# Performance work log

Measured on AMD Instinct MI355X. Metric: run time of the kernel, lower is better.

The kernel has to match this reference:

```python
import jax, jax.numpy as jnp
import numpy as np

N_DRUG = 50000
N_PROT = 50000
E = 1000000
H = 128

def setup_inputs() -> dict:
    key = jax.random.key(0)
    k1, k2, k3, k4, k5 = jax.random.split(key, 5)
    z_drug = jax.random.normal(k1, (N_DRUG, H), dtype=jnp.float32)
    z_protein = jax.random.normal(k2, (N_PROT, H), dtype=jnp.float32)
    edge_label_index = jax.random.randint(k3, (2, E), 0, N_DRUG, dtype=jnp.int64)
    # Linear params (Kaiming-ish scale)
    W1 = jax.random.normal(k4, (H, 2 * H), dtype=jnp.float32) / np.sqrt(2 * H)
    b1 = jnp.zeros((H,), dtype=jnp.float32)
    W2 = jax.random.normal(k5, (1, H), dtype=jnp.float32) / np.sqrt(H)
    b2 = jnp.zeros((1,), dtype=jnp.float32)
    return {"z_drug": z_drug, "z_protein": z_protein,
            "edge_label_index": edge_label_index,
            "W1": W1, "b1": b1, "W2": W2, "b2": b2}

def reference(z_drug, z_protein, edge_label_index, W1, b1, W2, b2):
    row, col = edge_label_index[0], edge_label_index[1]
    # gather node embeddings along edges, concat -> [E, 2H]
    z = jnp.concatenate([z_drug[row], z_protein[col]], axis=-1)
    h = jax.nn.relu(jnp.einsum('eh,oh->eo', z, W1) + b1)  # [E, H]
    out = jnp.einsum('eh,oh->eo', h, W2) + b2             # [E, 1]
    return out.reshape(-1)
```

## Files before the change

### kernel.cpp

```cpp
#include <hip/hip_runtime.h>


typedef __attribute__((ext_vector_type(8))) short bhalf8;
typedef __attribute__((ext_vector_type(4))) float f32x4;
typedef _Float16 half2_t __attribute__((ext_vector_type(2)));

__device__ __forceinline__ unsigned bfr(float f) {
    unsigned u = __builtin_bit_cast(unsigned, f);
    return (u + 0x7fffu + ((u >> 16) & 1u)) >> 16;
}
__device__ __forceinline__ unsigned pk2(float a, float b) {
    return bfr(a) | (bfr(b) << 16);
}

#define SH_STRIDE 132

__global__ __launch_bounds__(512) void hprepq_kernel(
    const float* __restrict__ zd, const float* __restrict__ zp,
    const float* __restrict__ W1, const float* __restrict__ b1,
    unsigned char* __restrict__ Hd, unsigned char* __restrict__ Hp,
    float* __restrict__ scD, float* __restrict__ scP,
    int Nd, int Np, int nbd)
{
    __shared__ __align__(16) char smem[64 * SH_STRIDE * 4];
    short* sZ = (short*)smem;
    float* sH = (float*)smem;

    const bool isP = (int)blockIdx.x >= nbd;
    const float* z = isP ? zp : zd;
    unsigned char* H = isP ? Hp : Hd;
    float* sc = isP ? scP : scD;
    const int N    = isP ? Np : Nd;
    const int koff = isP ? 128 : 0;
    const int blk  = isP ? blockIdx.x - nbd : blockIdx.x;

    const int tid  = threadIdx.x;
    const int wave = tid >> 6;
    const int lane = tid & 63;
    const int l15  = lane & 15;
    const int lhi  = lane >> 4;
    const int ocol = wave * 16 + l15;

    bhalf8 bfrag[4];
    #pragma unroll
    for (int ks = 0; ks < 4; ++ks) {
        const float4* src = (const float4*)(W1 + ocol * 256 + koff + ks * 32 + lhi * 8);
        float4 p = src[0], q = src[1];
        bhalf8 f;
        f[0] = (short)bfr(p.x); f[1] = (short)bfr(p.y);
        f[2] = (short)bfr(p.z); f[3] = (short)bfr(p.w);
        f[4] = (short)bfr(q.x); f[5] = (short)bfr(q.y);
        f[6] = (short)bfr(q.z); f[7] = (short)bfr(q.w);
        bfrag[ks] = f;
    }
    const float bias = isP ? 0.0f : b1[ocol];
    const int r0 = blk * 64;

    {
        const int rl = tid >> 3;
        const int grow = min(r0 + rl, N - 1);
        const float4* zr = (const float4*)(z + (size_t)grow * 128);
        #pragma unroll
        for (int q = 0; q < 4; ++q) {
            const int s = (tid & 7) + q * 8;
            float4 v = zr[s];
            uint2 w; w.x = pk2(v.x, v.y); w.y = pk2(v.z, v.w);
            int byte = (rl * 256 + s * 8) ^ ((rl & 7) << 4);
            *(uint2*)((char*)sZ + byte) = w;
        }
    }
    __syncthreads();

    f32x4 acc[4] = {{0.f,0.f,0.f,0.f},{0.f,0.f,0.f,0.f},
                    {0.f,0.f,0.f,0.f},{0.f,0.f,0.f,0.f}};
    #pragma unroll
    for (int ks = 0; ks < 4; ++ks) {
        #pragma unroll
        for (int rt = 0; rt < 4; ++rt) {
            const int row = rt * 16 + l15;
            int byte = (row * 256 + ks * 64 + lhi * 16) ^ ((row & 7) << 4);
            bhalf8 af = *(const bhalf8*)((const char*)sZ + byte);
            acc[rt] = __builtin_amdgcn_mfma_f32_16x16x32_bf16(af, bfrag[ks], acc[rt], 0, 0, 0);
        }
    }
    __syncthreads();

    #pragma unroll
    for (int rt = 0; rt < 4; ++rt) {
        #pragma unroll
        for (int i = 0; i < 4; ++i) {
            const int row = rt * 16 + lhi * 4 + i;
            sH[row * SH_STRIDE + ocol] = acc[rt][i] + bias;
        }
    }
    __syncthreads();

    {
        const int qrow = tid >> 3;
        const int k    = tid & 7;
        float4 v4[4];
        float mx = 0.0f;
        #pragma unroll
        for (int j = 0; j < 4; ++j) {
            v4[j] = *(const float4*)(sH + qrow * SH_STRIDE + k * 16 + j * 4);
            mx = fmaxf(mx, fmaxf(fmaxf(fabsf(v4[j].x), fabsf(v4[j].y)),
                                 fmaxf(fabsf(v4[j].z), fabsf(v4[j].w))));
        }
        mx = fmaxf(mx, __shfl_xor(mx, 1, 64));
        mx = fmaxf(mx, __shfl_xor(mx, 2, 64));
        mx = fmaxf(mx, __shfl_xor(mx, 4, 64));
        const float inv = 127.0f / fmaxf(mx, 1e-20f);
        uint4 o;
        unsigned ob[4];
        #pragma unroll
        for (int j = 0; j < 4; ++j) {
            int a0 = __float2int_rn(v4[j].x * inv);
            int a1 = __float2int_rn(v4[j].y * inv);
            int a2 = __float2int_rn(v4[j].z * inv);
            int a3 = __float2int_rn(v4[j].w * inv);
            ob[j] = ((unsigned)(a0 & 0xff) | ((unsigned)(a1 & 0xff) << 8) |
                     ((unsigned)(a2 & 0xff) << 16) | ((unsigned)(a3 & 0xff) << 24))
                    ^ 0x80808080u;
        }
        o.x = ob[0]; o.y = ob[1]; o.z = ob[2]; o.w = ob[3];
        const int grow = r0 + qrow;
        if (grow < N) {
            *(uint4*)(H + (size_t)grow * 128 + k * 16) = o;
            if (k == 0) sc[grow] = mx * (1.0f / 127.0f);
        }
    }
}

__global__ __launch_bounds__(256, 4) void edgeq_kernel(
    const unsigned char* __restrict__ Hd, const unsigned char* __restrict__ Hp,
    const float* __restrict__ scD, const float* __restrict__ scP,
    const int* __restrict__ eli, const float* __restrict__ W2,
    const float* __restrict__ b2, float* __restrict__ out, int E)
{
    const int sub = threadIdx.x & 7;
    const int grp = threadIdx.x >> 3;
    half2_t w2h[8];
    #pragma unroll
    for (int j = 0; j < 8; ++j) {
        float2 w = ((const float2*)W2)[sub * 8 + j];
        w2h[j][0] = (_Float16)w.x; w2h[j][1] = (_Float16)w.y;
    }
    const float b2v = b2[0];
    const half2_t c1152 = { (_Float16)1152.0f, (_Float16)1152.0f };

    const int EPB = 32 * 4;
    const int step = gridDim.x * EPB;
    int base = blockIdx.x * EPB;
    if (base >= E) return;

    int row[4], col[4];
    #pragma unroll
    for (int u = 0; u < 4; ++u) {
        const int e = base + grp * 4 + u;
        row[u] = (e < E) ? eli[e] : 0;
        col[u] = (e < E) ? eli[E + e] : 0;
    }

    for (; base < E; base += step) {
        uint4 qd[4], qp[4];
        float sdc[4], r[4];
        #pragma unroll
        for (int u = 0; u < 4; ++u) {
            qd[u] = *(const uint4*)(Hd + (size_t)row[u] * 128 + sub * 16);
            qp[u] = *(const uint4*)(Hp + (size_t)col[u] * 128 + sub * 16);
            const float sd = scD[row[u]];
            const float sp = scP[col[u]];
            sdc[u] = fmaxf(sd, 1e-25f);
            r[u]   = sp * __builtin_amdgcn_rcpf(sdc[u]);
        }
        const int nb = base + step;
        if (nb < E) {
            #pragma unroll
            for (int u = 0; u < 4; ++u) {
                const int e = nb + grp * 4 + u;
                row[u] = (e < E) ? eli[e] : 0;
                col[u] = (e < E) ? eli[E + e] : 0;
            }
        }
        #pragma unroll
        for (int u = 0; u < 4; ++u) {
            const _Float16 rh = (_Float16)r[u];
            const half2_t ru2 = { rh, rh };
            float s = 0.f;
            const unsigned dws[4] = {qd[u].x, qd[u].y, qd[u].z, qd[u].w};
            const unsigned pws[4] = {qp[u].x, qp[u].y, qp[u].z, qp[u].w};
            #pragma unroll
            for (int j = 0; j < 4; ++j) {
                const unsigned dw = dws[j], pw = pws[j];
                half2_t d0 = __builtin_bit_cast(half2_t,
                    __builtin_amdgcn_perm(0x64646464u, dw, 0x04010400u)) - c1152;
                half2_t d1 = __builtin_bit_cast(half2_t,
                    __builtin_amdgcn_perm(0x64646464u, dw, 0x04030402u)) - c1152;
                half2_t p0 = __builtin_bit_cast(half2_t,
                    __builtin_amdgcn_perm(0x64646464u, pw, 0x04010400u)) - c1152;
                half2_t p1 = __builtin_bit_cast(half2_t,
                    __builtin_amdgcn_perm(0x64646464u, pw, 0x04030402u)) - c1152;
                half2_t t0 = __builtin_elementwise_max(
                    __builtin_elementwise_fma(ru2, p0, d0), (half2_t){0, 0});
                half2_t t1 = __builtin_elementwise_max(
                    __builtin_elementwise_fma(ru2, p1, d1), (half2_t){0, 0});
                s = __builtin_amdgcn_fdot2(t0, w2h[j * 2],     s, false);
                s = __builtin_amdgcn_fdot2(t1, w2h[j * 2 + 1], s, false);
            }
            s += __shfl_xor(s, 1, 64);
            s += __shfl_xor(s, 2, 64);
            s += __shfl_xor(s, 4, 64);
            const int e = base + grp * 4 + u;
            if (sub == 0 && e < E) out[e] = fmaf(s, sdc[u], b2v);
        }
    }
}

#define TE 64
__global__ __launch_bounds__(512, 4) void ec_fallback(
    const float* __restrict__ zd, const float* __restrict__ zp,
    const int* __restrict__ eli, const float* __restrict__ W1,
    const float* __restrict__ b1, const float* __restrict__ W2,
    const float* __restrict__ b2, float* __restrict__ out,
    int E, int nTiles)
{
    __shared__ __align__(16) short sZ[TE * 256];
    __shared__ float sPart[8][TE];
    const int tid  = threadIdx.x;
    const int wave = tid >> 6;
    const int lane = tid & 63;
    const int l15  = lane & 15;
    const int lhi  = lane >> 4;
    const int ocol = wave * 16 + l15;
    bhalf8 bfrag[8];
    #pragma unroll
    for (int ks = 0; ks < 8; ++ks) {
        const float4* src = (const float4*)(W1 + ocol * 256 + ks * 32 + lhi * 8);
        float4 p = src[0], q = src[1];
        bhalf8 f;
        f[0] = (short)bfr(p.x); f[1] = (short)bfr(p.y);
        f[2] = (short)bfr(p.z); f[3] = (short)bfr(p.w);
        f[4] = (short)bfr(q.x); f[5] = (short)bfr(q.y);
        f[6] = (short)bfr(q.z); f[7] = (short)bfr(q.w);
        bfrag[ks] = f;
    }
    const float b1v = b1[ocol];
    const float w2v = W2[ocol];
    const float b2v = b2[0];
    const int slot = tid >> 5;
    const int lane32 = tid & 31;
    for (int tile = blockIdx.x; tile < nTiles; tile += gridDim.x) {
        const int base = tile * TE;
        __syncthreads();
        #pragma unroll
        for (int r = 0; r < 4; ++r) {
            const int e  = slot * 4 + r;
            const int eg = base + e;
            int drow = 0, pcol = 0;
            if (eg < E) { drow = eli[eg]; pcol = eli[E + eg]; }
            float4 v = ((const float4*)(zd + (size_t)drow * 128))[lane32];
            float4 u = ((const float4*)(zp + (size_t)pcol * 128))[lane32];
            int byte0 = (e * 512 + lane32 * 8) ^ ((e & 7) << 4);
            uint2 pv; pv.x = pk2(v.x, v.y); pv.y = pk2(v.z, v.w);
            *(uint2*)((char*)sZ + byte0) = pv;
            int byte1 = (e * 512 + 256 + lane32 * 8) ^ ((e & 7) << 4);
            uint2 pu; pu.x = pk2(u.x, u.y); pu.y = pk2(u.z, u.w);
            *(uint2*)((char*)sZ + byte1) = pu;
        }
        __syncthreads();
        f32x4 acc[4] = {{0.f,0.f,0.f,0.f},{0.f,0.f,0.f,0.f},
                        {0.f,0.f,0.f,0.f},{0.f,0.f,0.f,0.f}};
        #pragma unroll
        for (int ks = 0; ks < 8; ++ks) {
            const int kb = (ks * 32 + lhi * 8) * 2;
            #pragma unroll
            for (int rt = 0; rt < 4; ++rt) {
                const int row = rt * 16 + l15;
                int byte = (row * 512 + kb) ^ ((row & 7) << 4);
                bhalf8 af = *(const bhalf8*)((const char*)sZ + byte);
                acc[rt] = __builtin_amdgcn_mfma_f32_16x16x32_bf16(af, bfrag[ks], acc[rt], 0, 0, 0);
            }
        }
        #pragma unroll
        for (int rt = 0; rt < 4; ++rt) {
            #pragma unroll
            for (int i = 0; i < 4; ++i) {
                float v = acc[rt][i] + b1v;
                v = fmaxf(v, 0.0f) * w2v;
                v += __shfl_xor(v, 1, 64);
                v += __shfl_xor(v, 2, 64);
                v += __shfl_xor(v, 4, 64);
                v += __shfl_xor(v, 8, 64);
                if (l15 == 0) sPart[wave][rt * 16 + lhi * 4 + i] = v;
            }
        }
        __syncthreads();
        if (tid < TE) {
            const int eg = base + tid;
            if (eg < E) {
                float s = b2v;
                #pragma unroll
                for (int w = 0; w < 8; ++w) s += sPart[w][tid];
                out[eg] = s;
            }
        }
    }
}

extern "C" void kernel_launch(void* const* d_in, const int* in_sizes, int n_in,
                              void* d_out, int out_size, void* d_ws, size_t ws_size,
                              hipStream_t stream) {
    const float* zd = (const float*)d_in[0];
    const float* zp = (const float*)d_in[1];
    const int*   eli = (const int*)d_in[2];
    const float* W1 = (const float*)d_in[3];
    const float* b1 = (const float*)d_in[4];
    const float* W2 = (const float*)d_in[5];
    const float* b2 = (const float*)d_in[6];
    float* out = (float*)d_out;

    const int E  = in_sizes[2] / 2;
    const int nd = in_sizes[0];
    const int np = in_sizes[1];
    const int Nd = nd / 128, Np = np / 128;
    const int nbd = (Nd + 63) / 64, nbp = (Np + 63) / 64;

    const size_t offHp = (size_t)Nd * 128;
    const size_t offSd = (offHp + (size_t)Np * 128 + 15) & ~(size_t)15;
    const size_t offSp = offSd + (size_t)Nd * sizeof(float);
    const size_t need  = offSp + (size_t)Np * sizeof(float);

    if (ws_size >= need) {
        unsigned char* Hd = (unsigned char*)d_ws;
        unsigned char* Hp = Hd + offHp;
        float* scD = (float*)((char*)d_ws + offSd);
        float* scP = (float*)((char*)d_ws + offSp);
        hipLaunchKernelGGL(hprepq_kernel, dim3(nbd + nbp), dim3(512), 0, stream,
                           zd, zp, W1, b1, Hd, Hp, scD, scP, Nd, Np, nbd);
        hipLaunchKernelGGL(edgeq_kernel, dim3(4096), dim3(256), 0, stream,
                           Hd, Hp, scD, scP, eli, W2, b2, out, E);
    } else {
        const int nTiles = (E + TE - 1) / TE;
        hipLaunchKernelGGL(ec_fallback, dim3(2048), dim3(512), 0, stream,
                           zd, zp, eli, W1, b1, W2, b2, out, E, nTiles);
    }
}
```

Before: 57.91 us.

## Restructure prep kernel to quantize in registers and deepen edge gather batching

The node-projection kernel now runs 4 waves per block, and each wave computes two 16-column tiles, so every A fragment read from LDS feeds two MFMAs. Per-row absmax is found with shuffles plus LDS atomicMax instead of staging the fp32 tile in shared memory. Quantized bytes go into a swizzled LDS buffer and are written out with coalesced 16-byte stores. The edge kernel now handles 8 edges per thread group instead of 4, issues all gathers before the scale loads, and lowers its occupancy hint to 3, trading more registers for more memory-level parallelism.

```diff
diff --git a/kernel.cpp b/kernel.cpp
--- a/kernel.cpp
+++ b/kernel.cpp
@@ -13,18 +13,16 @@
     return bfr(a) | (bfr(b) << 16);
 }
 
-#define SH_STRIDE 132
-
-__global__ __launch_bounds__(512) void hprepq_kernel(
+__global__ __launch_bounds__(256) void hprepq_kernel(
     const float* __restrict__ zd, const float* __restrict__ zp,
     const float* __restrict__ W1, const float* __restrict__ b1,
     unsigned char* __restrict__ Hd, unsigned char* __restrict__ Hp,
     float* __restrict__ scD, float* __restrict__ scP,
     int Nd, int Np, int nbd)
 {
-    __shared__ __align__(16) char smem[64 * SH_STRIDE * 4];
-    short* sZ = (short*)smem;
-    float* sH = (float*)smem;
+    __shared__ __align__(16) short sZ[64 * 128];
+    __shared__ __align__(16) unsigned char sQ[64 * 128];
+    __shared__ int sMax[64];
 
     const bool isP = (int)blockIdx.x >= nbd;
     const float* z = isP ? zp : zd;
@@ -35,44 +33,57 @@
     const int blk  = isP ? blockIdx.x - nbd : blockIdx.x;
 
     const int tid  = threadIdx.x;
-    const int wave = tid >> 6;
+    const int w    = tid >> 6;
     const int lane = tid & 63;
     const int l15  = lane & 15;
     const int lhi  = lane >> 4;
-    const int ocol = wave * 16 + l15;
-
-    bhalf8 bfrag[4];
-    #pragma unroll
-    for (int ks = 0; ks < 4; ++ks) {
-        const float4* src = (const float4*)(W1 + ocol * 256 + koff + ks * 32 + lhi * 8);
-        float4 p = src[0], q = src[1];
-        bhalf8 f;
-        f[0] = (short)bfr(p.x); f[1] = (short)bfr(p.y);
-        f[2] = (short)bfr(p.z); f[3] = (short)bfr(p.w);
-        f[4] = (short)bfr(q.x); f[5] = (short)bfr(q.y);
-        f[6] = (short)bfr(q.z); f[7] = (short)bfr(q.w);
-        bfrag[ks] = f;
-    }
-    const float bias = isP ? 0.0f : b1[ocol];
+
+    if (tid < 64) sMax[tid] = 0;
+
+    bhalf8 bfrag[2][4];
+    #pragma unroll
+    for (int ct = 0; ct < 2; ++ct) {
+        const int ocol = w * 32 + ct * 16 + l15;
+        #pragma unroll
+        for (int ks = 0; ks < 4; ++ks) {
+            const float4* src = (const float4*)(W1 + ocol * 256 + koff + ks * 32 + lhi * 8);
+            float4 p = src[0], q = src[1];
+            bhalf8 f;
+            f[0] = (short)bfr(p.x); f[1] = (short)bfr(p.y);
+            f[2] = (short)bfr(p.z); f[3] = (short)bfr(p.w);
+            f[4] = (short)bfr(q.x); f[5] = (short)bfr(q.y);
+            f[6] = (short)bfr(q.z); f[7] = (short)bfr(q.w);
+            bfrag[ct][ks] = f;
+        }
+    }
+    float biasv[2];
+    #pragma unroll
+    for (int ct = 0; ct < 2; ++ct)
+        biasv[ct] = isP ? 0.0f : b1[w * 32 + ct * 16 + l15];
+
     const int r0 = blk * 64;
 
     {
-        const int rl = tid >> 3;
+        const int rl = tid >> 2;
         const int grow = min(r0 + rl, N - 1);
         const float4* zr = (const float4*)(z + (size_t)grow * 128);
         #pragma unroll
-        for (int q = 0; q < 4; ++q) {
-            const int s = (tid & 7) + q * 8;
+        for (int q = 0; q < 8; ++q) {
+            const int s = (tid & 3) + q * 4;
             float4 v = zr[s];
-            uint2 w; w.x = pk2(v.x, v.y); w.y = pk2(v.z, v.w);
+            uint2 ww; ww.x = pk2(v.x, v.y); ww.y = pk2(v.z, v.w);
             int byte = (rl * 256 + s * 8) ^ ((rl & 7) << 4);
-            *(uint2*)((char*)sZ + byte) = w;
+            *(uint2*)((char*)sZ + byte) = ww;
         }
     }
     __syncthreads();
 
-    f32x4 acc[4] = {{0.f,0.f,0.f,0.f},{0.f,0.f,0.f,0.f},
-                    {0.f,0.f,0.f,0.f},{0.f,0.f,0.f,0.f}};
+    f32x4 acc[2][4];
+    #pragma unroll
+    for (int ct = 0; ct < 2; ++ct)
+        #pragma unroll
+        for (int rt = 0; rt < 4; ++rt) acc[ct][rt] = (f32x4){0.f, 0.f, 0.f, 0.f};
+
     #pragma unroll
     for (int ks = 0; ks < 4; ++ks) {
         #pragma unroll
@@ -80,7 +91,30 @@
             const int row = rt * 16 + l15;
             int byte = (row * 256 + ks * 64 + lhi * 16) ^ ((row & 7) << 4);
             bhalf8 af = *(const bhalf8*)((const char*)sZ + byte);
-            acc[rt] = __builtin_amdgcn_mfma_f32_16x16x32_bf16(af, bfrag[ks], acc[rt], 0, 0, 0);
+            #pragma unroll
+            for (int ct = 0; ct < 2; ++ct)
+                acc[ct][rt] = __builtin_amdgcn_mfma_f32_16x16x32_bf16(af, bfrag[ct][ks], acc[ct][rt], 0, 0, 0);
+        }
+    }
+
+    #pragma unroll
+    for (int ct = 0; ct < 2; ++ct)
+        #pragma unroll
+        for (int rt = 0; rt < 4; ++rt)
+            #pragma unroll
+            for (int i = 0; i < 4; ++i) acc[ct][rt][i] += biasv[ct];
+
+    #pragma unroll
+    for (int rt = 0; rt < 4; ++rt) {
+        #pragma unroll
+        for (int i = 0; i < 4; ++i) {
+            float m = fmaxf(fabsf(acc[0][rt][i]), fabsf(acc[1][rt][i]));
+            m = fmaxf(m, __shfl_xor(m, 1, 64));
+            m = fmaxf(m, __shfl_xor(m, 2, 64));
+            m = fmaxf(m, __shfl_xor(m, 4, 64));
+            m = fmaxf(m, __shfl_xor(m, 8, 64));
+            if (l15 == 0)
+                atomicMax(&sMax[rt * 16 + lhi * 4 + i], __float_as_int(m));
         }
     }
     __syncthreads();
@@ -90,48 +124,35 @@
         #pragma unroll
         for (int i = 0; i < 4; ++i) {
             const int row = rt * 16 + lhi * 4 + i;
-            sH[row * SH_STRIDE + ocol] = acc[rt][i] + bias;
+            const float mx = __int_as_float(sMax[row]);
+            const float inv = 127.0f * __builtin_amdgcn_rcpf(fmaxf(mx, 1e-20f));
+            #pragma unroll
+            for (int ct = 0; ct < 2; ++ct) {
+                const int col = w * 32 + ct * 16 + l15;
+                int qv = __float2int_rn(acc[ct][rt][i] * inv);
+                sQ[row * 128 + (col ^ (lhi << 4))] = (unsigned char)((qv & 0xff) ^ 0x80);
+            }
+            if (w == 0 && l15 == 0) {
+                const int grow = r0 + row;
+                if (grow < N) sc[grow] = mx * (1.0f / 127.0f);
+            }
         }
     }
     __syncthreads();
 
-    {
-        const int qrow = tid >> 3;
-        const int k    = tid & 7;
-        float4 v4[4];
-        float mx = 0.0f;
-        #pragma unroll
-        for (int j = 0; j < 4; ++j) {
-            v4[j] = *(const float4*)(sH + qrow * SH_STRIDE + k * 16 + j * 4);
-            mx = fmaxf(mx, fmaxf(fmaxf(fabsf(v4[j].x), fabsf(v4[j].y)),
-                                 fmaxf(fabsf(v4[j].z), fabsf(v4[j].w))));
-        }
-        mx = fmaxf(mx, __shfl_xor(mx, 1, 64));
-        mx = fmaxf(mx, __shfl_xor(mx, 2, 64));
-        mx = fmaxf(mx, __shfl_xor(mx, 4, 64));
-        const float inv = 127.0f / fmaxf(mx, 1e-20f);
-        uint4 o;
-        unsigned ob[4];
-        #pragma unroll
-        for (int j = 0; j < 4; ++j) {
-            int a0 = __float2int_rn(v4[j].x * inv);
-            int a1 = __float2int_rn(v4[j].y * inv);
-            int a2 = __float2int_rn(v4[j].z * inv);
-            int a3 = __float2int_rn(v4[j].w * inv);
-            ob[j] = ((unsigned)(a0 & 0xff) | ((unsigned)(a1 & 0xff) << 8) |
-                     ((unsigned)(a2 & 0xff) << 16) | ((unsigned)(a3 & 0xff) << 24))
-                    ^ 0x80808080u;
-        }
-        o.x = ob[0]; o.y = ob[1]; o.z = ob[2]; o.w = ob[3];
-        const int grow = r0 + qrow;
-        if (grow < N) {
-            *(uint4*)(H + (size_t)grow * 128 + k * 16) = o;
-            if (k == 0) sc[grow] = mx * (1.0f / 127.0f);
-        }
-    }
-}
-
-__global__ __launch_bounds__(256, 4) void edgeq_kernel(
+    #pragma unroll
+    for (int j = 0; j < 2; ++j) {
+        const int chunk = tid + j * 256;
+        const int row = chunk >> 3;
+        const int b   = chunk & 7;
+        const int bs  = b ^ ((row >> 2) & 3);
+        uint4 v = *(const uint4*)(sQ + row * 128 + bs * 16);
+        const int grow = r0 + row;
+        if (grow < N) *(uint4*)(H + (size_t)grow * 128 + b * 16) = v;
+    }
+}
+
+__global__ __launch_bounds__(256, 3) void edgeq_kernel(
     const unsigned char* __restrict__ Hd, const unsigned char* __restrict__ Hp,
     const float* __restrict__ scD, const float* __restrict__ scP,
     const int* __restrict__ eli, const float* __restrict__ W2,
@@ -142,32 +163,35 @@
     half2_t w2h[8];
     #pragma unroll
     for (int j = 0; j < 8; ++j) {
-        float2 w = ((const float2*)W2)[sub * 8 + j];
-        w2h[j][0] = (_Float16)w.x; w2h[j][1] = (_Float16)w.y;
+        float2 ww = ((const float2*)W2)[sub * 8 + j];
+        w2h[j][0] = (_Float16)ww.x; w2h[j][1] = (_Float16)ww.y;
     }
     const float b2v = b2[0];
     const half2_t c1152 = { (_Float16)1152.0f, (_Float16)1152.0f };
 
-    const int EPB = 32 * 4;
+    const int EPB = 32 * 8;
     const int step = gridDim.x * EPB;
     int base = blockIdx.x * EPB;
     if (base >= E) return;
 
-    int row[4], col[4];
-    #pragma unroll
-    for (int u = 0; u < 4; ++u) {
-        const int e = base + grp * 4 + u;
+    int row[8], col[8];
+    #pragma unroll
+    for (int u = 0; u < 8; ++u) {
+        const int e = base + grp * 8 + u;
         row[u] = (e < E) ? eli[e] : 0;
         col[u] = (e < E) ? eli[E + e] : 0;
     }
 
     for (; base < E; base += step) {
-        uint4 qd[4], qp[4];
-        float sdc[4], r[4];
-        #pragma unroll
-        for (int u = 0; u < 4; ++u) {
+        uint4 qd[8], qp[8];
+        float sdc[8], r[8];
+        #pragma unroll
+        for (int u = 0; u < 8; ++u) {
             qd[u] = *(const uint4*)(Hd + (size_t)row[u] * 128 + sub * 16);
             qp[u] = *(const uint4*)(Hp + (size_t)col[u] * 128 + sub * 16);
+        }
+        #pragma unroll
+        for (int u = 0; u < 8; ++u) {
             const float sd = scD[row[u]];
             const float sp = scP[col[u]];
             sdc[u] = fmaxf(sd, 1e-25f);
@@ -176,14 +200,14 @@
         const int nb = base + step;
         if (nb < E) {
             #pragma unroll
-            for (int u = 0; u < 4; ++u) {
-                const int e = nb + grp * 4 + u;
+            for (int u = 0; u < 8; ++u) {
+                const int e = nb + grp * 8 + u;
                 row[u] = (e < E) ? eli[e] : 0;
                 col[u] = (e < E) ? eli[E + e] : 0;
             }
         }
         #pragma unroll
-        for (int u = 0; u < 4; ++u) {
+        for (int u = 0; u < 8; ++u) {
             const _Float16 rh = (_Float16)r[u];
             const half2_t ru2 = { rh, rh };
             float s = 0.f;
@@ -210,7 +234,7 @@
             s += __shfl_xor(s, 1, 64);
             s += __shfl_xor(s, 2, 64);
             s += __shfl_xor(s, 4, 64);
-            const int e = base + grp * 4 + u;
+            const int e = base + grp * 8 + u;
             if (sub == 0 && e < E) out[e] = fmaf(s, sdc[u], b2v);
         }
     }
@@ -335,7 +359,7 @@
         unsigned char* Hp = Hd + offHp;
         float* scD = (float*)((char*)d_ws + offSd);
         float* scP = (float*)((char*)d_ws + offSp);
-        hipLaunchKernelGGL(hprepq_kernel, dim3(nbd + nbp), dim3(512), 0, stream,
+        hipLaunchKernelGGL(hprepq_kernel, dim3(nbd + nbp), dim3(256), 0, stream,
                            zd, zp, W1, b1, Hd, Hp, scD, scP, Nd, Np, nbd);
         hipLaunchKernelGGL(edgeq_kernel, dim3(4096), dim3(256), 0, stream,
                            Hd, Hp, scD, scP, eli, W2, b2, out, E);
```

Result: slower. 78.06 us (+34.8%).
